# Kernel tuning notes

Hardware: AMD Instinct MI355X
Metric: run time of the kernel (lower is better)

## Reference

```python
import jax, jax.numpy as jnp
import numpy as np

B, T, IN, H = 16, 4096, 512, 512


def gru_layer(x, W_ih, W_hh, b_ih, b_hh):
    """Single-layer batch_first GRU, torch gate ordering (r, z, n), h0 = 0.
    x: [B, T, IN]; W_ih: [3H, IN]; W_hh: [3H, H]; b_ih, b_hh: [3H].
    Returns outputs [B, T, H]."""
    Bn = x.shape[0]
    Hn = W_hh.shape[1]
    # input-side gate pre-activations computed once as a big GEMM
    xg = jnp.einsum('bti,gi->btg', x, W_ih) + b_ih  # [B, T, 3H]

    def step(h, xg_t):
        hg = h @ W_hh.T + b_hh  # [B, 3H]
        xr, xz, xn = jnp.split(xg_t, 3, axis=-1)
        hr, hz, hn = jnp.split(hg, 3, axis=-1)
        r = jax.nn.sigmoid(xr + hr)
        z = jax.nn.sigmoid(xz + hz)
        n = jnp.tanh(xn + r * hn)
        h_new = (1.0 - z) * n + z * h
        return h_new, h_new

    h0 = jnp.zeros((Bn, Hn), dtype=x.dtype)
    _, ys = jax.lax.scan(step, h0, jnp.swapaxes(xg, 0, 1))  # [T, B, H]
    return jnp.swapaxes(ys, 0, 1)


def setup_inputs() -> dict:
    key = jax.random.key(0)
    ks = jax.random.split(key, 9)
    s = 1.0 / np.sqrt(H)  # torch GRU init scale
    x = jax.random.normal(ks[0], (B, T, IN), dtype=jnp.float32)
    W_ih1 = jax.random.uniform(ks[1], (3 * H, IN), jnp.float32, -s, s)
    W_hh1 = jax.random.uniform(ks[2], (3 * H, H), jnp.float32, -s, s)
    b_ih1 = jax.random.uniform(ks[3], (3 * H,), jnp.float32, -s, s)
    b_hh1 = jax.random.uniform(ks[4], (3 * H,), jnp.float32, -s, s)
    W_ih2 = jax.random.uniform(ks[5], (3 * H, H), jnp.float32, -s, s)
    W_hh2 = jax.random.uniform(ks[6], (3 * H, H), jnp.float32, -s, s)
    b_ih2 = jax.random.uniform(ks[7], (3 * H,), jnp.float32, -s, s)
    b_hh2 = jax.random.uniform(ks[8], (3 * H,), jnp.float32, -s, s)
    return {"x": x, "W_ih1": W_ih1, "W_hh1": W_hh1, "b_ih1": b_ih1, "b_hh1": b_hh1,
            "W_ih2": W_ih2, "W_hh2": W_hh2, "b_ih2": b_ih2, "b_hh2": b_hh2}


def reference(x, W_ih1, W_hh1, b_ih1, b_hh1, W_ih2, W_hh2, b_ih2, b_hh2):
    y = gru_layer(x, W_ih1, W_hh1, b_ih1, b_hh1)  # rnn1
    z = gru_layer(y, W_ih2, W_hh2, b_ih2, b_hh2)  # rnn2
    return z + y  # residual skip around second GRU
```

## Files before the change

kernel.cpp:

```cpp
#include <hip/hip_runtime.h>
#include <hip/hip_bf16.h>


namespace {

constexpr int BATCH = 16;
constexpr int SEQ   = 4096;
constexpr int HD    = 512;
constexpr int NWG_L = 32;
constexpr int SLICE = 16;
constexpr int RING  = 8;
constexpr int BLK   = 6 * 64;

typedef short bf16x8 __attribute__((ext_vector_type(8)));
typedef float f32x4  __attribute__((ext_vector_type(4)));

__device__ __forceinline__ unsigned short f2bf(float f) {
  unsigned u = __float_as_uint(f);
  return (unsigned short)((u + 0x7fffu + ((u >> 16) & 1u)) >> 16);
}
__device__ __forceinline__ float bf2f(unsigned short s) {
  return __uint_as_float(((unsigned)s) << 16);
}

__device__ __forceinline__ void wait_ge(const unsigned* f, unsigned tgt) {
  while (__hip_atomic_load(f, __ATOMIC_RELAXED, __HIP_MEMORY_SCOPE_AGENT) < tgt) {}
}

#define MFMA16(a, b, c) __builtin_amdgcn_mfma_f32_16x16x32_bf16((a), (b), (c), 0, 0, 0)

__global__ __launch_bounds__(BLK, 1) void gru2_kernel(
    const float* __restrict__ x,
    const float* __restrict__ Wih1, const float* __restrict__ Whh1,
    const float* __restrict__ bih1, const float* __restrict__ bhh1,
    const float* __restrict__ Wih2, const float* __restrict__ Whh2,
    const float* __restrict__ bih2, const float* __restrict__ bhh2,
    float* __restrict__ out,
    unsigned* flags,
    unsigned short* ring)
{
  const int wg    = blockIdx.x;
  const int layer = wg >> 5;
  const int g     = wg & 31;
  const int tid   = threadIdx.x;
  const int w     = tid >> 6;
  const int lane  = tid & 63;
  const int nidx  = lane & 15;
  const int kgrp  = lane >> 4;

  __shared__ float gate_buf[6][16][16];
  __shared__ float h_own[16][16];

  const float* Wih = layer ? Wih2 : Wih1;
  const float* Whh = layer ? Whh2 : Whh1;
  const float* bih = layer ? bih2 : bih1;
  const float* bhh = layer ? bhh2 : bhh1;

  unsigned* flags1    = flags;
  unsigned* flags2    = flags + 32;
  unsigned* flags_own = layer ? flags2 : flags1;

  const unsigned short* ring1 = ring;
  unsigned short* ring_own = ring + (size_t)layer * (RING * BATCH * HD);

  if (tid < 256) h_own[tid >> 4][tid & 15] = 0.f;

  const int gate = (w < 3) ? w : (w - 3);
  const float* Wmat = (w < 3) ? Wih : Whh;
  const float* wrow = Wmat + ((size_t)gate * HD + (size_t)g * SLICE + nidx) * HD + kgrp * 8;
  bf16x8 bfrag[16];
  #pragma unroll
  for (int kk = 0; kk < 16; ++kk) {
    const float* p = wrow + kk * 32;
    bf16x8 f;
    #pragma unroll
    for (int i = 0; i < 8; ++i) f[i] = (short)f2bf(p[i]);
    bfrag[kk] = f;
  }

  float bi_r = 0, bi_z = 0, bi_n = 0, bh_r = 0, bh_z = 0, bh_n = 0;
  if (tid < 256) {
    int u = g * SLICE + (tid & 15);
    bi_r = bih[u]; bi_z = bih[HD + u]; bi_n = bih[2 * HD + u];
    bh_r = bhh[u]; bh_z = bhh[HD + u]; bh_n = bhh[2 * HD + u];
  }
  __syncthreads();

  for (int t = 0; t < SEQ; ++t) {
    f32x4 ac0 = {0.f,0.f,0.f,0.f}, ac1 = {0.f,0.f,0.f,0.f};
    f32x4 ac2 = {0.f,0.f,0.f,0.f}, ac3 = {0.f,0.f,0.f,0.f};

    if (w < 3) {
      if (layer == 0) {
        const float* px = x + ((size_t)nidx * SEQ + t) * HD + kgrp * 8;
        #pragma unroll
        for (int kk = 0; kk < 16; ++kk) {
          const float* p = px + kk * 32;
          bf16x8 a;
          #pragma unroll
          for (int i = 0; i < 8; ++i) a[i] = (short)f2bf(p[i]);
          if ((kk & 3) == 0)      ac0 = MFMA16(a, bfrag[kk], ac0);
          else if ((kk & 3) == 1) ac1 = MFMA16(a, bfrag[kk], ac1);
          else if ((kk & 3) == 2) ac2 = MFMA16(a, bfrag[kk], ac2);
          else                    ac3 = MFMA16(a, bfrag[kk], ac3);
        }
      } else {
        if (lane < 32) wait_ge(&flags1[lane], (unsigned)(t + 1));
        __builtin_amdgcn_fence(__ATOMIC_ACQUIRE, "agent");
        const unsigned short* py =
            ring1 + ((size_t)(t & (RING - 1)) * BATCH + nidx) * HD + kgrp * 8;
        #pragma unroll
        for (int kk = 0; kk < 16; ++kk) {
          bf16x8 a = *(const bf16x8*)(py + kk * 32);
          if ((kk & 3) == 0)      ac0 = MFMA16(a, bfrag[kk], ac0);
          else if ((kk & 3) == 1) ac1 = MFMA16(a, bfrag[kk], ac1);
          else if ((kk & 3) == 2) ac2 = MFMA16(a, bfrag[kk], ac2);
          else                    ac3 = MFMA16(a, bfrag[kk], ac3);
        }
      }
    } else {
      if (t > 0) {
        if (lane < 32) {
          wait_ge(&flags_own[lane], (unsigned)t);
        } else if (layer == 0 && t >= RING) {
          wait_ge(&flags2[lane - 32], (unsigned)(t - RING + 1));
        }
        __builtin_amdgcn_fence(__ATOMIC_ACQUIRE, "agent");
        const unsigned short* ph =
            ring_own + ((size_t)((t - 1) & (RING - 1)) * BATCH + nidx) * HD + kgrp * 8;
        #pragma unroll
        for (int kk = 0; kk < 16; ++kk) {
          bf16x8 a = *(const bf16x8*)(ph + kk * 32);
          if ((kk & 3) == 0)      ac0 = MFMA16(a, bfrag[kk], ac0);
          else if ((kk & 3) == 1) ac1 = MFMA16(a, bfrag[kk], ac1);
          else if ((kk & 3) == 2) ac2 = MFMA16(a, bfrag[kk], ac2);
          else                    ac3 = MFMA16(a, bfrag[kk], ac3);
        }
      }
    }

    f32x4 acc = (ac0 + ac1) + (ac2 + ac3);
    #pragma unroll
    for (int j = 0; j < 4; ++j) gate_buf[w][kgrp * 4 + j][nidx] = acc[j];
    __syncthreads();

    if (tid < 256) {
      const int b = tid >> 4, u = tid & 15;
      float rp = gate_buf[0][b][u] + bi_r + gate_buf[3][b][u] + bh_r;
      float zp = gate_buf[1][b][u] + bi_z + gate_buf[4][b][u] + bh_z;
      float xn = gate_buf[2][b][u] + bi_n;
      float hn = gate_buf[5][b][u] + bh_n;
      float r = 1.f / (1.f + __expf(-rp));
      float z = 1.f / (1.f + __expf(-zp));
      float n = tanhf(xn + r * hn);
      float hp = h_own[b][u];
      float hv = (1.f - z) * n + z * hp;
      h_own[b][u] = hv;
      ring_own[((size_t)(t & (RING - 1)) * BATCH + b) * HD + g * SLICE + u] = f2bf(hv);
      if (layer == 1) {
        float y = bf2f(ring1[((size_t)(t & (RING - 1)) * BATCH + b) * HD + g * SLICE + u]);
        out[((size_t)b * SEQ + t) * HD + g * SLICE + u] = hv + y;
      }
    }
    __syncthreads();
    if (tid == 0) {
      __builtin_amdgcn_fence(__ATOMIC_RELEASE, "agent");
      __hip_atomic_store(&flags_own[g], (unsigned)(t + 1),
                         __ATOMIC_RELAXED, __HIP_MEMORY_SCOPE_AGENT);
    }
  }
}

}

extern "C" void kernel_launch(void* const* d_in, const int* in_sizes, int n_in,
                              void* d_out, int out_size, void* d_ws, size_t ws_size,
                              hipStream_t stream) {
  const float* x    = (const float*)d_in[0];
  const float* Wih1 = (const float*)d_in[1];
  const float* Whh1 = (const float*)d_in[2];
  const float* bih1 = (const float*)d_in[3];
  const float* bhh1 = (const float*)d_in[4];
  const float* Wih2 = (const float*)d_in[5];
  const float* Whh2 = (const float*)d_in[6];
  const float* bih2 = (const float*)d_in[7];
  const float* bhh2 = (const float*)d_in[8];

  unsigned* flags = (unsigned*)d_ws;
  unsigned short* ring = (unsigned short*)((char*)d_ws + 1024);

  hipMemsetAsync(d_ws, 0, 1024, stream);

  gru2_kernel<<<dim3(2 * NWG_L), dim3(BLK), 0, stream>>>(
      x, Wih1, Whh1, bih1, bhh1, Wih2, Whh2, bih2, bhh2,
      (float*)d_out, flags, ring);
}
```

Before: 37.12 ms.

## Replace per-workgroup flags with atomic counters and cache-bypassing ring loads/stores

Replaces the per-workgroup flag arrays with one atomic counter per layer, incremented via fetch_add, so waiting becomes a single polled address instead of 32 lanes each polling a flag. Acquire/release fences are removed; ring reads and writes now use sc0 sc1 global loads/stores with explicit vmcnt waits so data is coherent at device scope without fences. Ring stores are packed into dword pairs via shuffles, and the layer-2 residual read is packed the same way. The layer-0 input wave now does the ring-overflow wait on layer 2's counter. Correctness relies on the store-then-waitcnt ordering before the relaxed atomic increment, and all waves now spin on one hot counter address.

```diff
diff --git a/kernel.cpp b/kernel.cpp
--- a/kernel.cpp
+++ b/kernel.cpp
@@ -23,8 +23,13 @@
   return __uint_as_float(((unsigned)s) << 16);
 }
 
-__device__ __forceinline__ void wait_ge(const unsigned* f, unsigned tgt) {
-  while (__hip_atomic_load(f, __ATOMIC_RELAXED, __HIP_MEMORY_SCOPE_AGENT) < tgt) {}
+__device__ __forceinline__ void wait_cnt_ge(const unsigned* c, unsigned tgt) {
+  while (__hip_atomic_load(c, __ATOMIC_RELAXED, __HIP_MEMORY_SCOPE_AGENT) < tgt) {}
+}
+
+__device__ __forceinline__ void ld_frag_sc(bf16x8* dst, const unsigned short* p) {
+  asm volatile("global_load_dwordx4 %0, %1, off sc0 sc1"
+               : "=v"(*dst) : "v"(p) : "memory");
 }
 
 #define MFMA16(a, b, c) __builtin_amdgcn_mfma_f32_16x16x32_bf16((a), (b), (c), 0, 0, 0)
@@ -36,7 +41,7 @@
     const float* __restrict__ Wih2, const float* __restrict__ Whh2,
     const float* __restrict__ bih2, const float* __restrict__ bhh2,
     float* __restrict__ out,
-    unsigned* flags,
+    unsigned* cnt,
     unsigned short* ring)
 {
   const int wg    = blockIdx.x;
@@ -56,9 +61,9 @@
   const float* bih = layer ? bih2 : bih1;
   const float* bhh = layer ? bhh2 : bhh1;
 
-  unsigned* flags1    = flags;
-  unsigned* flags2    = flags + 32;
-  unsigned* flags_own = layer ? flags2 : flags1;
+  unsigned* cnt1 = cnt;
+  unsigned* cnt2 = cnt + 1;
+  unsigned* cnt_own = layer ? cnt2 : cnt1;
 
   const unsigned short* ring1 = ring;
   unsigned short* ring_own = ring + (size_t)layer * (RING * BATCH * HD);
@@ -104,37 +109,40 @@
           else if ((kk & 3) == 2) ac2 = MFMA16(a, bfrag[kk], ac2);
           else                    ac3 = MFMA16(a, bfrag[kk], ac3);
         }
+        if (t >= RING) wait_cnt_ge(cnt2, 32u * (unsigned)(t - RING + 1));
       } else {
-        if (lane < 32) wait_ge(&flags1[lane], (unsigned)(t + 1));
-        __builtin_amdgcn_fence(__ATOMIC_ACQUIRE, "agent");
+        wait_cnt_ge(cnt1, 32u * (unsigned)(t + 1));
         const unsigned short* py =
             ring1 + ((size_t)(t & (RING - 1)) * BATCH + nidx) * HD + kgrp * 8;
+        bf16x8 afr[16];
+        #pragma unroll
+        for (int kk = 0; kk < 16; ++kk) ld_frag_sc(&afr[kk], py + kk * 32);
+        asm volatile("s_waitcnt vmcnt(0)" ::: "memory");
+        __builtin_amdgcn_sched_barrier(0);
         #pragma unroll
         for (int kk = 0; kk < 16; ++kk) {
-          bf16x8 a = *(const bf16x8*)(py + kk * 32);
-          if ((kk & 3) == 0)      ac0 = MFMA16(a, bfrag[kk], ac0);
-          else if ((kk & 3) == 1) ac1 = MFMA16(a, bfrag[kk], ac1);
-          else if ((kk & 3) == 2) ac2 = MFMA16(a, bfrag[kk], ac2);
-          else                    ac3 = MFMA16(a, bfrag[kk], ac3);
+          if ((kk & 3) == 0)      ac0 = MFMA16(afr[kk], bfrag[kk], ac0);
+          else if ((kk & 3) == 1) ac1 = MFMA16(afr[kk], bfrag[kk], ac1);
+          else if ((kk & 3) == 2) ac2 = MFMA16(afr[kk], bfrag[kk], ac2);
+          else                    ac3 = MFMA16(afr[kk], bfrag[kk], ac3);
         }
       }
     } else {
       if (t > 0) {
-        if (lane < 32) {
-          wait_ge(&flags_own[lane], (unsigned)t);
-        } else if (layer == 0 && t >= RING) {
-          wait_ge(&flags2[lane - 32], (unsigned)(t - RING + 1));
-        }
-        __builtin_amdgcn_fence(__ATOMIC_ACQUIRE, "agent");
+        wait_cnt_ge(cnt_own, 32u * (unsigned)t);
         const unsigned short* ph =
             ring_own + ((size_t)((t - 1) & (RING - 1)) * BATCH + nidx) * HD + kgrp * 8;
+        bf16x8 afr[16];
+        #pragma unroll
+        for (int kk = 0; kk < 16; ++kk) ld_frag_sc(&afr[kk], ph + kk * 32);
+        asm volatile("s_waitcnt vmcnt(0)" ::: "memory");
+        __builtin_amdgcn_sched_barrier(0);
         #pragma unroll
         for (int kk = 0; kk < 16; ++kk) {
-          bf16x8 a = *(const bf16x8*)(ph + kk * 32);
-          if ((kk & 3) == 0)      ac0 = MFMA16(a, bfrag[kk], ac0);
-          else if ((kk & 3) == 1) ac1 = MFMA16(a, bfrag[kk], ac1);
-          else if ((kk & 3) == 2) ac2 = MFMA16(a, bfrag[kk], ac2);
-          else                    ac3 = MFMA16(a, bfrag[kk], ac3);
+          if ((kk & 3) == 0)      ac0 = MFMA16(afr[kk], bfrag[kk], ac0);
+          else if ((kk & 3) == 1) ac1 = MFMA16(afr[kk], bfrag[kk], ac1);
+          else if ((kk & 3) == 2) ac2 = MFMA16(afr[kk], bfrag[kk], ac2);
+          else                    ac3 = MFMA16(afr[kk], bfrag[kk], ac3);
         }
       }
     }
@@ -146,6 +154,13 @@
 
     if (tid < 256) {
       const int b = tid >> 4, u = tid & 15;
+      unsigned ypk = 0;
+      const unsigned short* pyr =
+          ring1 + ((size_t)(t & (RING - 1)) * BATCH + b) * HD + g * SLICE + (u & ~1);
+      if (layer == 1 && (u & 1) == 0) {
+        asm volatile("global_load_dword %0, %1, off sc0 sc1"
+                     : "=v"(ypk) : "v"(pyr) : "memory");
+      }
       float rp = gate_buf[0][b][u] + bi_r + gate_buf[3][b][u] + bh_r;
       float zp = gate_buf[1][b][u] + bi_z + gate_buf[4][b][u] + bh_z;
       float xn = gate_buf[2][b][u] + bi_n;
@@ -156,17 +171,26 @@
       float hp = h_own[b][u];
       float hv = (1.f - z) * n + z * hp;
       h_own[b][u] = hv;
-      ring_own[((size_t)(t & (RING - 1)) * BATCH + b) * HD + g * SLICE + u] = f2bf(hv);
+      unsigned hb = (unsigned)f2bf(hv);
+      unsigned nb = (unsigned)__shfl_down((int)hb, 1);
+      if ((u & 1) == 0) {
+        unsigned pk = (hb & 0xffffu) | (nb << 16);
+        unsigned short* pr =
+            ring_own + ((size_t)(t & (RING - 1)) * BATCH + b) * HD + g * SLICE + u;
+        asm volatile("global_store_dword %0, %1, off sc0 sc1"
+                     :: "v"(pr), "v"(pk) : "memory");
+      }
+      asm volatile("s_waitcnt vmcnt(0)" ::: "memory");
+      __builtin_amdgcn_sched_barrier(0);
       if (layer == 1) {
-        float y = bf2f(ring1[((size_t)(t & (RING - 1)) * BATCH + b) * HD + g * SLICE + u]);
+        unsigned pk2 = (unsigned)__shfl((int)ypk, (lane & ~1));
+        float y = bf2f((unsigned short)((u & 1) ? (pk2 >> 16) : (pk2 & 0xffffu)));
         out[((size_t)b * SEQ + t) * HD + g * SLICE + u] = hv + y;
       }
     }
     __syncthreads();
     if (tid == 0) {
-      __builtin_amdgcn_fence(__ATOMIC_RELEASE, "agent");
-      __hip_atomic_store(&flags_own[g], (unsigned)(t + 1),
-                         __ATOMIC_RELAXED, __HIP_MEMORY_SCOPE_AGENT);
+      __hip_atomic_fetch_add(cnt_own, 1u, __ATOMIC_RELAXED, __HIP_MEMORY_SCOPE_AGENT);
     }
   }
 }
@@ -186,12 +210,12 @@
   const float* bih2 = (const float*)d_in[7];
   const float* bhh2 = (const float*)d_in[8];
 
-  unsigned* flags = (unsigned*)d_ws;
+  unsigned* cnt = (unsigned*)d_ws;
   unsigned short* ring = (unsigned short*)((char*)d_ws + 1024);
 
   hipMemsetAsync(d_ws, 0, 1024, stream);
 
   gru2_kernel<<<dim3(2 * NWG_L), dim3(BLK), 0, stream>>>(
       x, Wih1, Whh1, bih1, bhh1, Wih2, Whh2, bih2, bhh2,
-      (float*)d_out, flags, ring);
-}
+      (float*)d_out, cnt, ring);
+}
```

Result: faster. 35.50 ms (-4.4%).
